# Kernel optimization log

Hardware: AMD Instinct MI355X
Metric: run time of the kernel (lower is better)

## Reference

```python
import jax, jax.numpy as jnp
import numpy as np

COMMITMENT_COST = 0.25


def setup_inputs() -> dict:
    key = jax.random.key(0)
    k1, k2 = jax.random.split(key)
    inputs = jax.random.normal(k1, (8, 1024, 512), dtype=jnp.float32)
    codebook = jax.random.normal(k2, (8192, 512), dtype=jnp.float32)
    return {"inputs": inputs, "codebook": codebook}


def reference(inputs, codebook):
    B, S, D = inputs.shape
    flat = inputs.reshape(-1, D)  # [N, D]
    distances = (
        jnp.sum(flat * flat, axis=1, keepdims=True)
        + jnp.sum(codebook * codebook, axis=1)
        - 2.0 * flat @ codebook.T
    )
    encoding_indices = jnp.argmin(distances, axis=1)  # [N] int
    min_distances = jnp.min(distances, axis=1)  # [N]
    quantized = codebook[encoding_indices].reshape(inputs.shape)  # [B,S,D]
    # straight-through estimator
    quantized_st = inputs + jax.lax.stop_gradient(quantized - inputs)
    # mse losses with reduction='sum'; .detach() -> stop_gradient
    loss_vq = jnp.sum((quantized - jax.lax.stop_gradient(inputs)) ** 2)
    loss_commit = jnp.sum((inputs - jax.lax.stop_gradient(quantized)) ** 2)
    # non-EMA branch: loss = commitment_cost * loss_commit + loss_vq
    loss = loss_commit * COMMITMENT_COST + loss_vq
    return (
        quantized_st,
        loss,
        encoding_indices.reshape(B, S),
        min_distances.reshape(B, S),
        loss_commit,
    )
```

## Files before the change

### kernel.cpp

```cpp
#include <hip/hip_runtime.h>

typedef __attribute__((ext_vector_type(8)))  short short8;
typedef __attribute__((ext_vector_type(16))) float f32x16;
typedef unsigned short ushort_t;
typedef unsigned int uint32;

#define NROWS 8192
#define NCODE 8192
#define DIM   512

#define OUT_Q      0
#define OUT_LOSS   4194304
#define OUT_IDX    4194305
#define OUT_MIND   4202497
#define OUT_COMMIT 4210689

#define WS_ENORM  0
#define WS_PMIN   8192
#define WS_PIDX   73728
#define WS_LPART  147456
#define WS_BHI    150528
#define WS_BLO    2247680

__device__ inline uint32 bf16_rne(float f) {
    uint32 u = __float_as_uint(f);
    return (u + 0x7FFFu + ((u >> 16) & 1u)) >> 16;
}

__device__ inline void gload16(const ushort_t* g, ushort_t* l) {
    __builtin_amdgcn_global_load_lds(
        (const __attribute__((address_space(1))) void*)g,
        (__attribute__((address_space(3))) void*)l, 16, 0, 0);
}

__global__ __launch_bounds__(256) void conv_kernel(const float* __restrict__ x,
                                                   const float* __restrict__ cb,
                                                   ushort_t* __restrict__ ahi,
                                                   ushort_t* __restrict__ alo,
                                                   ushort_t* __restrict__ bhi,
                                                   ushort_t* __restrict__ blo,
                                                   float* __restrict__ enorm) {
    int gid  = blockIdx.x * 256 + threadIdx.x;
    bool isA = gid < 524288;
    int g    = isA ? gid : gid - 524288;
    int row  = g >> 6;
    int lane = g & 63;
    int k0   = lane * 8;
    const float* src = (isA ? x : cb) + (size_t)row * DIM + k0;
    float v[8];
    *(float4*)&v[0] = *(const float4*)src;
    *(float4*)&v[4] = *(const float4*)(src + 4);
    float s = 0.0f;
    uint32 h[8], l[8];
    #pragma unroll
    for (int i = 0; i < 8; ++i) {
        s += v[i] * v[i];
        h[i] = bf16_rne(v[i]);
        float hf = __uint_as_float(h[i] << 16);
        l[i] = bf16_rne(v[i] - hf);
    }
    int tile = (row >> 7) * 16 + (k0 >> 5);
    int rp = row & 127, kp = k0 & 31;
    int c  = (rp >> 5) * 2 + (kp >> 4);
    int L  = (rp & 31) + (((kp >> 3) & 1) << 5);
    size_t off = (size_t)tile * 4096 + c * 512 + L * 8;
    uint4 ph, pl;
    ph.x = h[0] | (h[1] << 16); ph.y = h[2] | (h[3] << 16);
    ph.z = h[4] | (h[5] << 16); ph.w = h[6] | (h[7] << 16);
    pl.x = l[0] | (l[1] << 16); pl.y = l[2] | (l[3] << 16);
    pl.z = l[4] | (l[5] << 16); pl.w = l[6] | (l[7] << 16);
    if (isA) {
        *(uint4*)(ahi + off) = ph;
        *(uint4*)(alo + off) = pl;
    } else {
        *(uint4*)(bhi + off) = ph;
        *(uint4*)(blo + off) = pl;
        #pragma unroll
        for (int o = 32; o > 0; o >>= 1) s += __shfl_down(s, o);
        if (lane == 0) enorm[row] = s;
    }
}

struct Frags { short8 ah[2]; short8 al[2]; short8 bh[4]; short8 bl[4]; };

__global__ __launch_bounds__(256, 2) void vq_mfma_kernel(
        const ushort_t* __restrict__ ahi, const ushort_t* __restrict__ alo,
        const ushort_t* __restrict__ bhi, const ushort_t* __restrict__ blo,
        const float* __restrict__ enorm,
        float* __restrict__ pmin, int* __restrict__ pidx) {
    __shared__ __align__(16) ushort_t smem[36864];

    const int tid  = threadIdx.x;
    const int wave = tid >> 6, lane = tid & 63;
    const int l31  = lane & 31, half = lane >> 5;
    const int q  = blockIdx.x;
    const int bx = (q & 7) * 8 + (q >> 6);
    const int by = (q >> 3) & 7;
    const int wr = wave >> 1;
    const int wc = wave & 1;
    const int wr2 = wr * 2, wc4 = wc * 4;
    const int l8 = lane * 8;

    f32x16 acc[2][4];
    #pragma unroll
    for (int i = 0; i < 2; ++i)
        #pragma unroll
        for (int j = 0; j < 4; ++j)
            #pragma unroll
            for (int r = 0; r < 16; ++r) acc[i][j][r] = 0.0f;

    float keys[32];
    #pragma unroll
    for (int i = 0; i < 32; ++i) keys[i] = 3.4e38f;

    auto stage = [&](int nn) {
        const int kb = nn & 31, kc = kb >> 1, k16 = kb & 1;
        const int ct = nn >> 5;
        ushort_t* S2 = smem + (nn % 3) * 12288;
        const int lo = (tid >> 6) * 1024 + (k16 << 9) + (tid & 63) * 8;
        const size_t at = ((size_t)bx * 16 + kc) << 12;
        gload16(ahi + at + lo, S2 + tid * 8);
        gload16(alo + at + lo, S2 + 2048 + tid * 8);
        const int c0 = by * 8 + ct * 2;
        const size_t bt0 = ((size_t)c0 * 16 + kc) << 12;
        const size_t bt1 = bt0 + ((size_t)16 << 12);
        gload16(bhi + bt0 + lo, S2 + 4096 + tid * 8);
        gload16(bhi + bt1 + lo, S2 + 6144 + tid * 8);
        gload16(blo + bt0 + lo, S2 + 8192 + tid * 8);
        gload16(blo + bt1 + lo, S2 + 10240 + tid * 8);
    };

#define RD(base) (*(const short8*)&Sr[(base) + l8])
#define MFMA8(A, B) do {                                                      \
    __builtin_amdgcn_s_setprio(1);                                            \
    _Pragma("unroll")                                                         \
    for (int ti = 0; ti < 2; ++ti)                                            \
        _Pragma("unroll")                                                     \
        for (int tj = 0; tj < 4; ++tj)                                        \
            acc[ti][tj] = __builtin_amdgcn_mfma_f32_32x32x16_bf16(            \
                (A)[ti], (B)[tj], acc[ti][tj], 0, 0, 0);                      \
    __builtin_amdgcn_s_setprio(0);                                            \
} while (0)

#define BODY(nn, CUR, NXT) do {                                               \
    if ((nn) + 2 < 128) {                                                     \
        stage((nn) + 2);                                                      \
        asm volatile("s_waitcnt vmcnt(6)" ::: "memory");                      \
    } else {                                                                  \
        asm volatile("s_waitcnt vmcnt(0)" ::: "memory");                      \
    }                                                                         \
    asm volatile("s_barrier" ::: "memory");                                   \
    __builtin_amdgcn_sched_barrier(0);                                        \
    const ushort_t* Sr = smem + (((nn) + 1) % 3) * 12288;                     \
    MFMA8(CUR.ah, CUR.bh);                                            \
    NXT.ah[0] = RD((wr2 + 0) * 512);                      \
    NXT.ah[1] = RD((wr2 + 1) * 512);                                          \
    NXT.bh[0] = RD(4096 + (wc4 + 0) * 512);                                   \
    NXT.bh[1] = RD(4096 + (wc4 + 1) * 512);                                   \
    NXT.bh[2] = RD(4096 + (wc4 + 2) * 512);                                   \
    NXT.bh[3] = RD(4096 + (wc4 + 3) * 512);                                   \
    MFMA8(CUR.ah, CUR.bl);                                            \
    NXT.bl[0] = RD(8192 + (wc4 + 0) * 512);               \
    NXT.bl[1] = RD(8192 + (wc4 + 1) * 512);                                   \
    NXT.bl[2] = RD(8192 + (wc4 + 2) * 512);                                   \
    NXT.bl[3] = RD(8192 + (wc4 + 3) * 512);                                   \
    NXT.al[0] = RD(2048 + (wr2 + 0) * 512);                                   \
    NXT.al[1] = RD(2048 + (wr2 + 1) * 512);                                   \
    MFMA8(CUR.al, CUR.bh);                                            \
    if (((nn) & 31) == 31) {                                                  \
        const int ct = (nn) >> 5;                                             \
        const int colbase = by * 1024 + ct * 256 + wc * 128;                  \
        _Pragma("unroll")                                                     \
        for (int tj = 0; tj < 4; ++tj) {                                      \
            const int ci = colbase + tj * 32 + l31;                           \
            const float en = enorm[ci];                                       \
            _Pragma("unroll")                                                 \
            for (int ti = 0; ti < 2; ++ti)                                    \
                _Pragma("unroll")                                             \
                for (int r = 0; r < 16; ++r) {                                \
                    float d = en - 2.0f * acc[ti][tj][r];                     \
                    float cand = __uint_as_float(                             \
                        (__float_as_uint(d) & 0xFFFFE000u) | (uint32)ci);     \
                    int s = ti * 16 + r;                                      \
                    if (cand < keys[s]) keys[s] = cand;                       \
                }                                                             \
        }                                                                     \
        _Pragma("unroll")                                                     \
        for (int i = 0; i < 2; ++i)                                           \
            _Pragma("unroll")                                                 \
            for (int j = 0; j < 4; ++j)                                       \
                _Pragma("unroll")                                             \
                for (int r = 0; r < 16; ++r) acc[i][j][r] = 0.0f;             \
    }                                                                         \
} while (0)

    Frags Fa, Fb;

    stage(0); stage(1);
    asm volatile("s_waitcnt vmcnt(6)" ::: "memory");
    __syncthreads();
    {
        const ushort_t* Sr = smem;
        Fa.ah[0] = RD((wr2 + 0) * 512);  Fa.ah[1] = RD((wr2 + 1) * 512);
        Fa.al[0] = RD(2048 + (wr2 + 0) * 512);
        Fa.al[1] = RD(2048 + (wr2 + 1) * 512);
        #pragma unroll
        for (int tj = 0; tj < 4; ++tj) {
            Fa.bh[tj] = RD(4096 + (wc4 + tj) * 512);
            Fa.bl[tj] = RD(8192 + (wc4 + tj) * 512);
        }
    }

    for (int n = 0; n < 128; n += 2) {
        BODY(n, Fa, Fb);
        BODY(n + 1, Fb, Fa);
    }

    __syncthreads();
    float* rd = (float*)smem;
    #pragma unroll
    for (int s = 0; s < 32; ++s) {
        float k = keys[s];
        #pragma unroll
        for (int m = 16; m > 0; m >>= 1) k = fminf(k, __shfl_xor(k, m));
        if (l31 == 0) {
            int r = s & 15;
            int row = wr * 64 + (s >> 4) * 32 + (r & 3) + 8 * (r >> 2) + 4 * half;
            rd[wc * 128 + row] = k;
        }
    }
    __syncthreads();
    if (tid < 128) {
        float k = fminf(rd[tid], rd[128 + tid]);
        size_t gr = (size_t)bx * 128 + tid;
        pmin[gr * 8 + by] = k;
        pidx[gr * 8 + by] = (int)(__float_as_uint(k) & 8191u);
    }
#undef RD
#undef MFMA8
#undef BODY
}

__global__ __launch_bounds__(256) void finish_kernel(const float* __restrict__ x,
                                                     const float* __restrict__ cb,
                                                     const float* __restrict__ pmin,
                                                     const int* __restrict__ pidx,
                                                     float* __restrict__ out_idx,
                                                     float* __restrict__ qout,
                                                     float* __restrict__ out_mind,
                                                     float* __restrict__ lpart) {
    __shared__ float sred[4];
    int row  = blockIdx.x * 4 + (threadIdx.x >> 6);
    int lane = threadIdx.x & 63;

    float d = (lane < 8) ? pmin[(size_t)row * 8 + lane] : 3.4e38f;
    int  ii = (lane < 8) ? pidx[(size_t)row * 8 + lane] : 0x7FFFFFFF;
    #pragma unroll
    for (int o = 4; o > 0; o >>= 1) {
        float d2 = __shfl_down(d, o);
        int   i2 = __shfl_down(ii, o);
        if (d2 < d || (d2 == d && i2 < ii)) { d = d2; ii = i2; }
    }
    int idx = __shfl(ii, 0);
    if (lane == 0) out_idx[row] = (float)idx;

    const float4* e4 = (const float4*)(cb + (size_t)idx * DIM);
    const float4* x4 = (const float4*)(x + (size_t)row * DIM);
    float4* q4 = (float4*)(qout + (size_t)row * DIM);
    float s = 0.0f;
    #pragma unroll
    for (int u = 0; u < 2; ++u) {
        float4 e  = e4[lane + u * 64];
        float4 xv = x4[lane + u * 64];
        q4[lane + u * 64] = e;
        float dx = xv.x - e.x, dy = xv.y - e.y, dz = xv.z - e.z, dw = xv.w - e.w;
        s += dx * dx + dy * dy + dz * dz + dw * dw;
    }
    #pragma unroll
    for (int o = 32; o > 0; o >>= 1) s += __shfl_down(s, o);
    if (lane == 0) { sred[threadIdx.x >> 6] = s; out_mind[row] = s; }
    __syncthreads();
    if (threadIdx.x == 0) lpart[blockIdx.x] = sred[0] + sred[1] + sred[2] + sred[3];
}

__global__ __launch_bounds__(256) void loss_kernel(const float* __restrict__ lpart,
                                                   float* __restrict__ out_loss,
                                                   float* __restrict__ out_commit) {
    __shared__ float sm[256];
    float s = 0.0f;
    for (int i = threadIdx.x; i < 2048; i += 256) s += lpart[i];
    sm[threadIdx.x] = s;
    __syncthreads();
    #pragma unroll
    for (int o = 128; o > 0; o >>= 1) {
        if (threadIdx.x < o) sm[threadIdx.x] += sm[threadIdx.x + o];
        __syncthreads();
    }
    if (threadIdx.x == 0) {
        *out_commit = sm[0];
        *out_loss   = 1.25f * sm[0];
    }
}

extern "C" void kernel_launch(void* const* d_in, const int* in_sizes, int n_in,
                              void* d_out, int out_size, void* d_ws, size_t ws_size,
                              hipStream_t stream) {
    const float* x  = (const float*)d_in[0];
    const float* cb = (const float*)d_in[1];
    float* out = (float*)d_out;
    float* ws  = (float*)d_ws;

    ushort_t* ahi = (ushort_t*)d_out;
    ushort_t* alo = (ushort_t*)d_out + 4194304;
    ushort_t* bhi = (ushort_t*)(ws + WS_BHI);
    ushort_t* blo = (ushort_t*)(ws + WS_BLO);
    float* enorm = ws + WS_ENORM;
    float* pmin  = ws + WS_PMIN;
    int*   pidx  = (int*)(ws + WS_PIDX);
    float* lpart = ws + WS_LPART;

    conv_kernel<<<4096, 256, 0, stream>>>(x, cb, ahi, alo, bhi, blo, enorm);
    vq_mfma_kernel<<<512, 256, 0, stream>>>(ahi, alo, bhi, blo, enorm, pmin, pidx);
    finish_kernel<<<NROWS / 4, 256, 0, stream>>>(x, cb, pmin, pidx,
                                                 out + OUT_IDX, out + OUT_Q,
                                                 out + OUT_MIND, lpart);
    loss_kernel<<<1, 256, 0, stream>>>(lpart, out + OUT_LOSS, out + OUT_COMMIT);
}
```

Baseline: 274.8 us.

## Drop LDS staging, load MFMA fragments directly from global, reduce argmin via 64-bit atomicMin

The GEMM kernel drops its triple-buffered LDS pipeline, barriers and async global-to-LDS loads. Each wave now loads its bf16 hi/lo fragments straight from global memory into registers, one step ahead. The block tiling changes to 256 rows by 512 codes, with each wave owning distinct rows. The argmin is reduced per wave with shuffles and merged across blocks with 64-bit atomicMin on packed sign-fixed distance and index keys, initialised in conv_kernel, which removes the finish-side partial reduction. The trade is that data reuse across waves through LDS is lost, so global and L2 traffic rises, and the atomics add contention.

Measured after the change: 327.6 us. 1.19x slower.

```diff
diff --git a/kernel.cpp b/kernel.cpp
--- a/kernel.cpp
+++ b/kernel.cpp
@@ -4,6 +4,7 @@
 typedef __attribute__((ext_vector_type(16))) float f32x16;
 typedef unsigned short ushort_t;
 typedef unsigned int uint32;
+typedef unsigned long long uint64;
 
 #define NROWS 8192
 #define NCODE 8192
@@ -16,8 +17,7 @@
 #define OUT_COMMIT 4210689
 
 #define WS_ENORM  0
-#define WS_PMIN   8192
-#define WS_PIDX   73728
+#define WS_KEYS   8192
 #define WS_LPART  147456
 #define WS_BHI    150528
 #define WS_BLO    2247680
@@ -25,12 +25,6 @@
 __device__ inline uint32 bf16_rne(float f) {
     uint32 u = __float_as_uint(f);
     return (u + 0x7FFFu + ((u >> 16) & 1u)) >> 16;
-}
-
-__device__ inline void gload16(const ushort_t* g, ushort_t* l) {
-    __builtin_amdgcn_global_load_lds(
-        (const __attribute__((address_space(1))) void*)g,
-        (__attribute__((address_space(3))) void*)l, 16, 0, 0);
 }
 
 __global__ __launch_bounds__(256) void conv_kernel(const float* __restrict__ x,
@@ -39,8 +33,10 @@
                                                    ushort_t* __restrict__ alo,
                                                    ushort_t* __restrict__ bhi,
                                                    ushort_t* __restrict__ blo,
-                                                   float* __restrict__ enorm) {
+                                                   float* __restrict__ enorm,
+                                                   uint64* __restrict__ keys) {
     int gid  = blockIdx.x * 256 + threadIdx.x;
+    if (gid < NROWS) keys[gid] = 0xFFFFFFFFFFFFFFFFull;
     bool isA = gid < 524288;
     int g    = isA ? gid : gid - 524288;
     int row  = g >> 6;
@@ -81,25 +77,21 @@
     }
 }
 
-struct Frags { short8 ah[2]; short8 al[2]; short8 bh[4]; short8 bl[4]; };
+struct Frag { short8 ah[2]; short8 al[2]; short8 bh[4]; short8 bl[4]; };
 
 __global__ __launch_bounds__(256, 2) void vq_mfma_kernel(
         const ushort_t* __restrict__ ahi, const ushort_t* __restrict__ alo,
         const ushort_t* __restrict__ bhi, const ushort_t* __restrict__ blo,
-        const float* __restrict__ enorm,
-        float* __restrict__ pmin, int* __restrict__ pidx) {
-    __shared__ __align__(16) ushort_t smem[36864];
-
+        const float* __restrict__ enorm, uint64* __restrict__ keys) {
     const int tid  = threadIdx.x;
     const int wave = tid >> 6, lane = tid & 63;
     const int l31  = lane & 31, half = lane >> 5;
-    const int q  = blockIdx.x;
-    const int bx = (q & 7) * 8 + (q >> 6);
-    const int by = (q >> 3) & 7;
-    const int wr = wave >> 1;
-    const int wc = wave & 1;
-    const int wr2 = wr * 2, wc4 = wc * 4;
-    const int l8 = lane * 8;
+    const int q   = blockIdx.x;
+    const int t   = q >> 3;
+    const int bx  = (q & 7) * 4 + (t >> 4);
+    const int by  = t & 15;
+    const int r32 = bx * 8 + wave * 2;
+    const int l8  = lane * 8;
 
     f32x16 acc[2][4];
     #pragma unroll
@@ -109,28 +101,25 @@
             #pragma unroll
             for (int r = 0; r < 16; ++r) acc[i][j][r] = 0.0f;
 
-    float keys[32];
-    #pragma unroll
-    for (int i = 0; i < 32; ++i) keys[i] = 3.4e38f;
-
-    auto stage = [&](int nn) {
-        const int kb = nn & 31, kc = kb >> 1, k16 = kb & 1;
-        const int ct = nn >> 5;
-        ushort_t* S2 = smem + (nn % 3) * 12288;
-        const int lo = (tid >> 6) * 1024 + (k16 << 9) + (tid & 63) * 8;
-        const size_t at = ((size_t)bx * 16 + kc) << 12;
-        gload16(ahi + at + lo, S2 + tid * 8);
-        gload16(alo + at + lo, S2 + 2048 + tid * 8);
-        const int c0 = by * 8 + ct * 2;
-        const size_t bt0 = ((size_t)c0 * 16 + kc) << 12;
-        const size_t bt1 = bt0 + ((size_t)16 << 12);
-        gload16(bhi + bt0 + lo, S2 + 4096 + tid * 8);
-        gload16(bhi + bt1 + lo, S2 + 6144 + tid * 8);
-        gload16(blo + bt0 + lo, S2 + 8192 + tid * 8);
-        gload16(blo + bt1 + lo, S2 + 10240 + tid * 8);
+    auto FOFF = [&](int rt, int kk) -> size_t {
+        return ((size_t)((rt >> 2) * 16 + (kk >> 1))) * 4096
+             + (size_t)(((rt & 3) * 2 + (kk & 1)) * 512) + l8;
     };
 
-#define RD(base) (*(const short8*)&Sr[(base) + l8])
+#define LOADF(F, nn) do {                                                     \
+    const int ct_ = (nn) >> 5, kk_ = (nn) & 31;                               \
+    (F).ah[0] = *(const short8*)&ahi[FOFF(r32,     kk_)];                     \
+    (F).ah[1] = *(const short8*)&ahi[FOFF(r32 + 1, kk_)];                     \
+    (F).al[0] = *(const short8*)&alo[FOFF(r32,     kk_)];                     \
+    (F).al[1] = *(const short8*)&alo[FOFF(r32 + 1, kk_)];                     \
+    _Pragma("unroll")                                                         \
+    for (int tj = 0; tj < 4; ++tj) {                                          \
+        const int c32 = by * 16 + ct_ * 4 + tj;                               \
+        (F).bh[tj] = *(const short8*)&bhi[FOFF(c32, kk_)];                    \
+        (F).bl[tj] = *(const short8*)&blo[FOFF(c32, kk_)];                    \
+    }                                                                         \
+} while (0)
+
 #define MFMA8(A, B) do {                                                      \
     __builtin_amdgcn_s_setprio(1);                                            \
     _Pragma("unroll")                                                         \
@@ -143,48 +132,41 @@
 } while (0)
 
 #define BODY(nn, CUR, NXT) do {                                               \
-    if ((nn) + 2 < 128) {                                                     \
-        stage((nn) + 2);                                                      \
-        asm volatile("s_waitcnt vmcnt(6)" ::: "memory");                      \
-    } else {                                                                  \
-        asm volatile("s_waitcnt vmcnt(0)" ::: "memory");                      \
-    }                                                                         \
-    asm volatile("s_barrier" ::: "memory");                                   \
-    __builtin_amdgcn_sched_barrier(0);                                        \
-    const ushort_t* Sr = smem + (((nn) + 1) % 3) * 12288;                     \
-    MFMA8(CUR.ah, CUR.bh);                                            \
-    NXT.ah[0] = RD((wr2 + 0) * 512);                      \
-    NXT.ah[1] = RD((wr2 + 1) * 512);                                          \
-    NXT.bh[0] = RD(4096 + (wc4 + 0) * 512);                                   \
-    NXT.bh[1] = RD(4096 + (wc4 + 1) * 512);                                   \
-    NXT.bh[2] = RD(4096 + (wc4 + 2) * 512);                                   \
-    NXT.bh[3] = RD(4096 + (wc4 + 3) * 512);                                   \
-    MFMA8(CUR.ah, CUR.bl);                                            \
-    NXT.bl[0] = RD(8192 + (wc4 + 0) * 512);               \
-    NXT.bl[1] = RD(8192 + (wc4 + 1) * 512);                                   \
-    NXT.bl[2] = RD(8192 + (wc4 + 2) * 512);                                   \
-    NXT.bl[3] = RD(8192 + (wc4 + 3) * 512);                                   \
-    NXT.al[0] = RD(2048 + (wr2 + 0) * 512);                                   \
-    NXT.al[1] = RD(2048 + (wr2 + 1) * 512);                                   \
-    MFMA8(CUR.al, CUR.bh);                                            \
+    if ((nn) + 1 < 128) LOADF(NXT, (nn) + 1);                                 \
+    MFMA8(CUR.ah, CUR.bh);                                                    \
+    MFMA8(CUR.ah, CUR.bl);                                                    \
+    MFMA8(CUR.al, CUR.bh);                                                    \
     if (((nn) & 31) == 31) {                                                  \
-        const int ct = (nn) >> 5;                                             \
-        const int colbase = by * 1024 + ct * 256 + wc * 128;                  \
-        _Pragma("unroll")                                                     \
-        for (int tj = 0; tj < 4; ++tj) {                                      \
-            const int ci = colbase + tj * 32 + l31;                           \
-            const float en = enorm[ci];                                       \
+        const int ct_ = (nn) >> 5;                                            \
+        const int colbase = by * 512 + ct_ * 128;                             \
+        float en[4];                                                          \
+        _Pragma("unroll")                                                     \
+        for (int tj = 0; tj < 4; ++tj) en[tj] = enorm[colbase + tj*32 + l31]; \
+        _Pragma("unroll")                                                     \
+        for (int ti = 0; ti < 2; ++ti)                                        \
             _Pragma("unroll")                                                 \
-            for (int ti = 0; ti < 2; ++ti)                                    \
+            for (int r = 0; r < 16; ++r) {                                    \
+                float bd = 3.4e38f; int bc = 0;                               \
                 _Pragma("unroll")                                             \
-                for (int r = 0; r < 16; ++r) {                                \
-                    float d = en - 2.0f * acc[ti][tj][r];                     \
-                    float cand = __uint_as_float(                             \
-                        (__float_as_uint(d) & 0xFFFFE000u) | (uint32)ci);     \
-                    int s = ti * 16 + r;                                      \
-                    if (cand < keys[s]) keys[s] = cand;                       \
+                for (int tj = 0; tj < 4; ++tj) {                              \
+                    float d = en[tj] - 2.0f * acc[ti][tj][r];                 \
+                    int ci = colbase + tj * 32 + l31;                         \
+                    if (d < bd) { bd = d; bc = ci; }                          \
                 }                                                             \
-        }                                                                     \
+                _Pragma("unroll")                                             \
+                for (int m = 1; m < 32; m <<= 1) {                            \
+                    float d2 = __shfl_xor(bd, m);                             \
+                    int   c2 = __shfl_xor(bc, m);                             \
+                    if (d2 < bd || (d2 == bd && c2 < bc)) { bd = d2; bc = c2;}\
+                }                                                             \
+                if (l31 == 0) {                                               \
+                    int row = bx * 256 + wave * 64 + ti * 32                  \
+                            + (r & 3) + 8 * (r >> 2) + 4 * half;              \
+                    uint32 u  = __float_as_uint(bd);                          \
+                    uint32 su = u ^ (0x80000000u | (uint32)((int)u >> 31));   \
+                    atomicMin(&keys[row], ((uint64)su << 32) | (uint32)bc);   \
+                }                                                             \
+            }                                                                 \
         _Pragma("unroll")                                                     \
         for (int i = 0; i < 2; ++i)                                           \
             _Pragma("unroll")                                                 \
@@ -194,57 +176,20 @@
     }                                                                         \
 } while (0)
 
-    Frags Fa, Fb;
-
-    stage(0); stage(1);
-    asm volatile("s_waitcnt vmcnt(6)" ::: "memory");
-    __syncthreads();
-    {
-        const ushort_t* Sr = smem;
-        Fa.ah[0] = RD((wr2 + 0) * 512);  Fa.ah[1] = RD((wr2 + 1) * 512);
-        Fa.al[0] = RD(2048 + (wr2 + 0) * 512);
-        Fa.al[1] = RD(2048 + (wr2 + 1) * 512);
-        #pragma unroll
-        for (int tj = 0; tj < 4; ++tj) {
-            Fa.bh[tj] = RD(4096 + (wc4 + tj) * 512);
-            Fa.bl[tj] = RD(8192 + (wc4 + tj) * 512);
-        }
-    }
-
+    Frag Fa, Fb;
+    LOADF(Fa, 0);
     for (int n = 0; n < 128; n += 2) {
         BODY(n, Fa, Fb);
         BODY(n + 1, Fb, Fa);
     }
-
-    __syncthreads();
-    float* rd = (float*)smem;
-    #pragma unroll
-    for (int s = 0; s < 32; ++s) {
-        float k = keys[s];
-        #pragma unroll
-        for (int m = 16; m > 0; m >>= 1) k = fminf(k, __shfl_xor(k, m));
-        if (l31 == 0) {
-            int r = s & 15;
-            int row = wr * 64 + (s >> 4) * 32 + (r & 3) + 8 * (r >> 2) + 4 * half;
-            rd[wc * 128 + row] = k;
-        }
-    }
-    __syncthreads();
-    if (tid < 128) {
-        float k = fminf(rd[tid], rd[128 + tid]);
-        size_t gr = (size_t)bx * 128 + tid;
-        pmin[gr * 8 + by] = k;
-        pidx[gr * 8 + by] = (int)(__float_as_uint(k) & 8191u);
-    }
-#undef RD
+#undef LOADF
 #undef MFMA8
 #undef BODY
 }
 
 __global__ __launch_bounds__(256) void finish_kernel(const float* __restrict__ x,
                                                      const float* __restrict__ cb,
-                                                     const float* __restrict__ pmin,
-                                                     const int* __restrict__ pidx,
+                                                     const uint64* __restrict__ keys,
                                                      float* __restrict__ out_idx,
                                                      float* __restrict__ qout,
                                                      float* __restrict__ out_mind,
@@ -253,15 +198,7 @@
     int row  = blockIdx.x * 4 + (threadIdx.x >> 6);
     int lane = threadIdx.x & 63;
 
-    float d = (lane < 8) ? pmin[(size_t)row * 8 + lane] : 3.4e38f;
-    int  ii = (lane < 8) ? pidx[(size_t)row * 8 + lane] : 0x7FFFFFFF;
-    #pragma unroll
-    for (int o = 4; o > 0; o >>= 1) {
-        float d2 = __shfl_down(d, o);
-        int   i2 = __shfl_down(ii, o);
-        if (d2 < d || (d2 == d && i2 < ii)) { d = d2; ii = i2; }
-    }
-    int idx = __shfl(ii, 0);
+    int idx = (int)(uint32)(keys[row] & 0xFFFFFFFFull);
     if (lane == 0) out_idx[row] = (float)idx;
 
     const float4* e4 = (const float4*)(cb + (size_t)idx * DIM);
@@ -314,14 +251,13 @@
     ushort_t* alo = (ushort_t*)d_out + 4194304;
     ushort_t* bhi = (ushort_t*)(ws + WS_BHI);
     ushort_t* blo = (ushort_t*)(ws + WS_BLO);
-    float* enorm = ws + WS_ENORM;
-    float* pmin  = ws + WS_PMIN;
-    int*   pidx  = (int*)(ws + WS_PIDX);
-    float* lpart = ws + WS_LPART;
-
-    conv_kernel<<<4096, 256, 0, stream>>>(x, cb, ahi, alo, bhi, blo, enorm);
-    vq_mfma_kernel<<<512, 256, 0, stream>>>(ahi, alo, bhi, blo, enorm, pmin, pidx);
-    finish_kernel<<<NROWS / 4, 256, 0, stream>>>(x, cb, pmin, pidx,
+    float*  enorm = ws + WS_ENORM;
+    uint64* keys  = (uint64*)(ws + WS_KEYS);
+    float*  lpart = ws + WS_LPART;
+
+    conv_kernel<<<4096, 256, 0, stream>>>(x, cb, ahi, alo, bhi, blo, enorm, keys);
+    vq_mfma_kernel<<<512, 256, 0, stream>>>(ahi, alo, bhi, blo, enorm, keys);
+    finish_kernel<<<NROWS / 4, 256, 0, stream>>>(x, cb, keys,
                                                  out + OUT_IDX, out + OUT_Q,
                                                  out + OUT_MIND, lpart);
     loss_kernel<<<1, 256, 0, stream>>>(lpart, out + OUT_LOSS, out + OUT_COMMIT);
```
